# Kernel optimization log

Hardware: AMD Instinct MI355X
Metric: run time of the kernel (lower is better)

Reference implementation:

```python
import jax, jax.numpy as jnp
import numpy as np

B, E, CIN, O = 2, 50000, 8, 128


def _mesh_conv(x, gemm, w, b):
    # MeshCNN MeshConv: x (B,C,E), gemm (B,E,4) neighbor indices, w (O,C,5), b (O,)
    # gather 4 GeMM neighbors per edge, build 5 symmetric features, 1x5 conv
    neigh = jax.vmap(lambda xb, gb: xb[:, gb])(x, gemm)  # (B,C,E,4)
    f1, f2, f3, f4 = neigh[..., 0], neigh[..., 1], neigh[..., 2], neigh[..., 3]
    G = jnp.stack([x, f1 + f3, f2 + f4, jnp.abs(f1 - f3), jnp.abs(f2 - f4)], axis=-1)  # (B,C,E,5)
    return jnp.einsum('bces,ocs->boe', G, w) + b[None, :, None]


def _inorm(x, eps=1e-5):
    # InstanceNorm (no affine, biased variance) over the edge dim, per (batch, channel)
    m = jnp.mean(x, axis=-1, keepdims=True)
    v = jnp.var(x, axis=-1, keepdims=True)
    return (x - m) * jax.lax.rsqrt(v + eps)


def _conv1(x, w, b):
    # 1x1 Conv1d: x (B,C,E), w (O,C)
    return jnp.einsum('bce,oc->boe', x, w) + b[None, :, None]


def setup_inputs() -> dict:
    key = jax.random.key(0)
    ks = jax.random.split(key, 16)

    def W(k, shape, fan):
        return jax.random.normal(k, shape, jnp.float32) * np.float32(1.0 / np.sqrt(fan))

    d = {}
    d['fe'] = jax.random.normal(ks[0], (B, CIN, E), jnp.float32)
    d['gemm'] = jax.random.randint(ks[1], (B, E, 4), 0, E)
    # first-stage MeshConvs: geometry branch (5 ch) and position branch (3 ch)
    d['w_e1'] = W(ks[2], (O, 5, 5), 25);       d['b_e1'] = jnp.zeros((O,), jnp.float32)
    d['w_p1'] = W(ks[3], (O, 3, 5), 15);       d['b_p1'] = jnp.zeros((O,), jnp.float32)
    # residual-block MeshConvs (blocks=1)
    d['w_e2'] = W(ks[4], (O, O, 5), O * 5);    d['b_e2'] = jnp.zeros((O,), jnp.float32)
    d['w_p2'] = W(ks[5], (O, O, 5), O * 5);    d['b_p2'] = jnp.zeros((O,), jnp.float32)
    # Attn(in_dim=O)
    d['wa'] = W(ks[6], (O // 4, O), O);        d['ba'] = jnp.zeros((O // 4,), jnp.float32)
    d['wb'] = W(ks[7], (O // 4, O), O);        d['bb'] = jnp.zeros((O // 4,), jnp.float32)
    d['wal'] = W(ks[8], (O // 2, O // 2), O // 2);  d['bal'] = jnp.zeros((O // 2,), jnp.float32)
    d['wbl'] = W(ks[9], (O // 2, O // 2), O // 2);  d['bbl'] = jnp.zeros((O // 2,), jnp.float32)
    d['wat'] = W(ks[10], (O // 2, O // 2, 5), O // 2 * 5); d['bat'] = jnp.zeros((O // 2,), jnp.float32)
    d['wbt'] = W(ks[11], (O // 2, O // 2, 5), O // 2 * 5); d['bbt'] = jnp.zeros((O // 2,), jnp.float32)
    d['waf'] = W(ks[12], (O, O), O);           d['baf'] = jnp.zeros((O,), jnp.float32)
    d['wbf'] = W(ks[13], (O, O), O);           d['bbf'] = jnp.zeros((O,), jnp.float32)
    return d


def reference(fe, gemm, w_e1, b_e1, w_p1, b_p1, w_e2, b_e2, w_p2, b_p2,
              wa, ba, wb, bb, wal, bal, wbl, bbl, wat, bat, wbt, bbt,
              waf, baf, wbf, bbf):
    # DownConv (8-channel input path): split into edge (5) and point (3) branches
    fe_e, fe_p = fe[:, :5, :], fe[:, 5:, :]
    x1_e = jax.nn.relu(_inorm(_mesh_conv(fe_e, gemm, w_e1, b_e1)))
    x2_e = jax.nn.relu(_inorm(_mesh_conv(x1_e, gemm, w_e2, b_e2)) + x1_e)
    x1_p = jax.nn.relu(_inorm(_mesh_conv(fe_p, gemm, w_p1, b_p1)))
    x2_p = jax.nn.relu(_inorm(_mesh_conv(x1_p, gemm, w_p2, b_p2)) + x1_p)
    # Attn fusion
    x_all = jnp.concatenate([_conv1(x2_e, wa, ba), _conv1(x2_p, wb, bb)], axis=1)  # (B, O/2, E)
    x_a_two = jnp.concatenate([_conv1(x_all, wal, bal), _mesh_conv(x_all, gemm, wat, bat)], axis=1)
    x_b_two = jnp.concatenate([_conv1(x_all, wbl, bbl), _mesh_conv(x_all, gemm, wbt, bbt)], axis=1)
    wA = jax.nn.sigmoid(_inorm(_conv1(x_a_two, waf, baf)))  # (B,O,E)
    wB = jax.nn.sigmoid(_inorm(_conv1(x_b_two, wbf, bbf)))
    weights = jax.nn.softmax(jnp.stack([wA, wB], axis=1), axis=1)  # (B,2,O,E)
    agg = x2_e * weights[:, 0] + x2_p * weights[:, 1]
    # x2_ep = cat(x2_e, x2_p); also emit the attention-fused combine (before_pool)
    return jnp.concatenate([x2_e, x2_p, agg], axis=1)  # (B, 3*O, E)
```

## Files before the change

kernel.cpp:

```cpp
#include <hip/hip_runtime.h>
#include <cstdio>
#include <math.h>


#define E_TOT 50000
#define B_TOT 2
#define TILE_E 64
#define NBLK ((E_TOT + TILE_E - 1) / TILE_E)

typedef _Float16 half_t;
typedef __attribute__((ext_vector_type(4))) _Float16 h4;
typedef __attribute__((ext_vector_type(8))) _Float16 h8;
typedef __attribute__((ext_vector_type(4))) float f32x4;

__device__ __forceinline__ float sigmoidf_(float x) {
    return 1.0f / (1.0f + __expf(-x));
}
__device__ __forceinline__ h8 habs8(h8 x) {
    union { h8 h; unsigned int u[4]; } v;
    v.h = x;
#pragma unroll
    for (int i = 0; i < 4; ++i) v.u[i] &= 0x7FFF7FFFu;
    return v.h;
}

#define OFF_W1E   0
#define OFF_W1P   8192
#define OFF_WTE2  16384
#define OFF_WTP2  98304
#define OFF_WHA   180224
#define OFF_WHB   221184
#define OFF_WTA   262144
#define OFF_WTB   266240
#define OFF_WTAF  270336
#define OFF_WTBF  286720
#define WARENA_N  303104

__global__ __launch_bounds__(256)
void wprep_k(half_t* __restrict__ wa_,
             const float* __restrict__ w_e1, const float* __restrict__ w_p1,
             const float* __restrict__ w_e2, const float* __restrict__ w_p2,
             const float* __restrict__ wat,  const float* __restrict__ wbt,
             const float* __restrict__ wa,   const float* __restrict__ wb,
             const float* __restrict__ wal,  const float* __restrict__ wbl,
             const float* __restrict__ waf,  const float* __restrict__ wbf)
{
    int idx = blockIdx.x * 256 + threadIdx.x;
    switch (blockIdx.y) {
    case 0: if (idx < 8192) { int o = idx >> 6, k = idx & 63, s = k >> 3, cc = k & 7;
            float v = (s < 5 && cc < 5) ? w_e1[o * 25 + cc * 5 + s] : 0.f;
            wa_[OFF_W1E + idx] = (half_t)v; } break;
    case 1: if (idx < 8192) { int o = idx >> 6, k = idx & 63, s = k >> 3, cc = k & 7;
            float v = (s < 5 && cc >= 5) ? w_p1[o * 15 + (cc - 5) * 5 + s] : 0.f;
            wa_[OFF_W1P + idx] = (half_t)v; } break;
    case 2: if (idx < 81920) { int o = idx / 640, r = idx % 640, s = r >> 7, c = r & 127;
            wa_[OFF_WTE2 + idx] = (half_t)w_e2[(o * 128 + c) * 5 + s]; } break;
    case 3: if (idx < 81920) { int o = idx / 640, r = idx % 640, s = r >> 7, c = r & 127;
            wa_[OFF_WTP2 + idx] = (half_t)w_p2[(o * 128 + c) * 5 + s]; } break;
    case 4: if (idx < 40960) { int o = idx / 320, r = idx % 320, s = r >> 6, c = r & 63;
            float v = (o < 64) ? (s == 0 ? wal[o * 64 + c] : 0.f)
                               : wat[((o - 64) * 64 + c) * 5 + s];
            wa_[OFF_WHA + idx] = (half_t)v; } break;
    case 5: if (idx < 40960) { int o = idx / 320, r = idx % 320, s = r >> 6, c = r & 63;
            float v = (o < 64) ? (s == 0 ? wbl[o * 64 + c] : 0.f)
                               : wbt[((o - 64) * 64 + c) * 5 + s];
            wa_[OFF_WHB + idx] = (half_t)v; } break;
    case 6: if (idx < 4096)  wa_[OFF_WTA  + idx] = (half_t)wa[idx];  break;
    case 7: if (idx < 4096)  wa_[OFF_WTB  + idx] = (half_t)wb[idx];  break;
    case 8: if (idx < 16384) wa_[OFF_WTAF + idx] = (half_t)waf[idx]; break;
    case 9: if (idx < 16384) wa_[OFF_WTBF + idx] = (half_t)wbf[idx]; break;
    }
}

__global__ __launch_bounds__(256)
void transpose_in_k(const float* __restrict__ fe, float* __restrict__ fet)
{
    int b = blockIdx.z;
    int e = blockIdx.x * 256 + threadIdx.x;
    if (e >= E_TOT) return;
    float v[8];
#pragma unroll
    for (int c = 0; c < 8; ++c)
        v[c] = fe[((long)b * 8 + c) * E_TOT + e];
    float4* dst = (float4*)&fet[((long)b * E_TOT + e) * 8];
    dst[0] = make_float4(v[0], v[1], v[2], v[3]);
    dst[1] = make_float4(v[4], v[5], v[6], v[7]);
}

__global__ __launch_bounds__(512)
void mesh1_both_k(const float* __restrict__ fet, const int* __restrict__ gemm,
                  const half_t* __restrict__ war,
                  const float* __restrict__ be1, const float* __restrict__ bp1,
                  half_t* __restrict__ tmpe, half_t* __restrict__ tmpp,
                  float* __restrict__ parte, float* __restrict__ partp)
{
    __shared__ h8 Gl[64 * 8];
    __shared__ int nidx[64][4];

    const int tid  = threadIdx.x;
    const int b    = blockIdx.y;
    const int e0   = blockIdx.x * TILE_E;
    const int lane = tid & 63;
    const int wv   = tid >> 6;
    const int l15  = lane & 15;
    const int kg   = lane >> 4;
    const int br   = wv >> 2;
    const int o0   = (wv & 3) * 32;

    const float* xb = fet + (long)b * E_TOT * 8;

    if (tid < 256) {
        int e = tid >> 2, s = tid & 3;
        int eg = e0 + e;
        nidx[e][s] = (eg < E_TOT) ? gemm[((long)b * E_TOT + eg) * 4 + s] : 0;
    }
    __syncthreads();

    {
        int e = tid >> 3, g = tid & 7;
        int eg = e0 + e;
        int se = (eg < E_TOT) ? eg : 0;
        h8 r;
        if (g == 0) {
            const float* p = xb + (long)se * 8;
            float4 v0 = *(const float4*)p, v1 = *(const float4*)(p + 4);
            r[0] = (half_t)v0.x; r[1] = (half_t)v0.y; r[2] = (half_t)v0.z; r[3] = (half_t)v0.w;
            r[4] = (half_t)v1.x; r[5] = (half_t)v1.y; r[6] = (half_t)v1.z; r[7] = (half_t)v1.w;
        } else if (g <= 4) {
            int ia = (g == 1 || g == 3) ? 0 : 1;
            const float* pa = xb + (long)nidx[e][ia] * 8;
            const float* pb = xb + (long)nidx[e][ia + 2] * 8;
            float4 a0 = *(const float4*)pa, a1 = *(const float4*)(pa + 4);
            float4 b0 = *(const float4*)pb, b1 = *(const float4*)(pb + 4);
            float aa[8] = {a0.x, a0.y, a0.z, a0.w, a1.x, a1.y, a1.z, a1.w};
            float bb[8] = {b0.x, b0.y, b0.z, b0.w, b1.x, b1.y, b1.z, b1.w};
            if (g <= 2) {
#pragma unroll
                for (int j = 0; j < 8; ++j) r[j] = (half_t)(aa[j] + bb[j]);
            } else {
#pragma unroll
                for (int j = 0; j < 8; ++j) r[j] = (half_t)fabsf(aa[j] - bb[j]);
            }
        } else {
#pragma unroll
            for (int j = 0; j < 8; ++j) r[j] = (half_t)0.f;
        }
        Gl[(e * 8 + g) ^ (e & 7)] = r;
    }
    __syncthreads();

    f32x4 acc[4][2];
#pragma unroll
    for (int mt = 0; mt < 4; ++mt)
#pragma unroll
        for (int nt = 0; nt < 2; ++nt)
#pragma unroll
            for (int j = 0; j < 4; ++j) acc[mt][nt][j] = 0.f;

    const half_t* wt = war + (br ? OFF_W1P : OFF_W1E);
#pragma unroll
    for (int ks = 0; ks < 2; ++ks) {
        h8 bw[2];
#pragma unroll
        for (int nt = 0; nt < 2; ++nt)
            bw[nt] = *(const h8*)(wt + (long)(o0 + nt * 16 + l15) * 64 + ks * 32 + kg * 8);
#pragma unroll
        for (int mt = 0; mt < 4; ++mt) {
            int row = mt * 16 + l15;
            h8 a = Gl[row * 8 + ((ks * 4 + kg) ^ (row & 7))];
#pragma unroll
            for (int nt = 0; nt < 2; ++nt)
                acc[mt][nt] = __builtin_amdgcn_mfma_f32_16x16x32_f16(a, bw[nt], acc[mt][nt], 0, 0, 0);
        }
    }

    const float* bias = br ? bp1 : be1;
    half_t* yb = (br ? tmpp : tmpe) + (long)b * E_TOT * 128;
    float* part = br ? partp : parte;
    float bv[2], s1[2], s2[2];
#pragma unroll
    for (int nt = 0; nt < 2; ++nt) {
        bv[nt] = bias[o0 + nt * 16 + l15];
        s1[nt] = 0.f; s2[nt] = 0.f;
    }
#pragma unroll
    for (int mt = 0; mt < 4; ++mt) {
        int ebase = e0 + mt * 16 + (kg << 2);
#pragma unroll
        for (int j = 0; j < 4; ++j) {
            if (ebase + j < E_TOT) {
#pragma unroll
                for (int nt = 0; nt < 2; ++nt) {
                    float v = acc[mt][nt][j] + bv[nt];
                    yb[(long)(ebase + j) * 128 + o0 + nt * 16 + l15] = (half_t)v;
                    s1[nt] += v; s2[nt] += v * v;
                }
            }
        }
    }
#pragma unroll
    for (int nt = 0; nt < 2; ++nt) {
        s1[nt] += __shfl_xor(s1[nt], 16); s1[nt] += __shfl_xor(s1[nt], 32);
        s2[nt] += __shfl_xor(s2[nt], 16); s2[nt] += __shfl_xor(s2[nt], 32);
    }
    if (lane < 16) {
        long pb = ((long)b * NBLK + blockIdx.x) * 128;
#pragma unroll
        for (int nt = 0; nt < 2; ++nt) {
            part[(pb + o0 + nt * 16 + lane) * 2 + 0] = s1[nt];
            part[(pb + o0 + nt * 16 + lane) * 2 + 1] = s2[nt];
        }
    }
}

__global__ __launch_bounds__(512)
void mesh2_k(const half_t* __restrict__ x1e, const half_t* __restrict__ x1p,
             const int* __restrict__ gemm, const half_t* __restrict__ war,
             const float* __restrict__ be, const float* __restrict__ bp,
             half_t* __restrict__ tmpe, half_t* __restrict__ tmpp,
             float* __restrict__ parte, float* __restrict__ partp)
{
    __shared__ h8 GlA[64 * 16];
    __shared__ h8 GlB[64 * 16];
    __shared__ int nidx[64][4];

    const int tid  = threadIdx.x;
    const int br   = blockIdx.y;
    const int b    = blockIdx.z;
    const int e0   = blockIdx.x * TILE_E;
    const int lane = tid & 63;
    const int wv   = tid >> 6;
    const int l15  = lane & 15;
    const int kg   = lane >> 4;
    const int o0   = wv * 16;

    const half_t* xb = (br ? x1p : x1e) + (long)b * E_TOT * 128;
    const half_t* wt = war + (br ? OFF_WTP2 : OFF_WTE2);

    if (tid < 256) {
        int e = tid >> 2, s = tid & 3;
        int eg = e0 + e;
        nidx[e][s] = (eg < E_TOT) ? gemm[((long)b * E_TOT + eg) * 4 + s] : 0;
    }

    auto stage_self = [&](h8* dst) {
#pragma unroll
        for (int t = 0; t < 2; ++t) {
            int q = t * 512 + tid;
            int e = q >> 4, c8 = q & 15;
            int eg = e0 + e;
            int se = (eg < E_TOT) ? eg : 0;
            dst[(e * 16 + c8) ^ (e & 7)] = *(const h8*)(xb + (long)se * 128 + c8 * 8);
        }
    };
    auto stage_pair = [&](h8* dstS, h8* dstD, int ia, int ib) {
#pragma unroll
        for (int t = 0; t < 2; ++t) {
            int q = t * 512 + tid;
            int e = q >> 4, c8 = q & 15;
            int na = nidx[e][ia], nb = nidx[e][ib];
            h8 a  = *(const h8*)(xb + (long)na * 128 + c8 * 8);
            h8 bq = *(const h8*)(xb + (long)nb * 128 + c8 * 8);
            int slot = (e * 16 + c8) ^ (e & 7);
            dstS[slot] = a + bq;
            dstD[slot] = habs8(a - bq);
        }
    };

    f32x4 acc[4];
#pragma unroll
    for (int mt = 0; mt < 4; ++mt)
#pragma unroll
        for (int j = 0; j < 4; ++j) acc[mt][j] = 0.f;

    auto compute_chunk = [&](const h8* buf, int s) {
#pragma unroll
        for (int ks = 0; ks < 4; ++ks) {
            h8 bw = *(const h8*)(wt + ((long)(o0 + l15) * 5 + s) * 128 + ks * 32 + kg * 8);
#pragma unroll
            for (int mt = 0; mt < 4; ++mt) {
                int row = mt * 16 + l15;
                h8 a = buf[row * 16 + ((ks * 4 + kg) ^ (row & 7))];
                acc[mt] = __builtin_amdgcn_mfma_f32_16x16x32_f16(a, bw, acc[mt], 0, 0, 0);
            }
        }
    };

    stage_self(GlA);
    __syncthreads();
    compute_chunk(GlA, 0);
    __syncthreads();
    stage_pair(GlA, GlB, 0, 2);
    __syncthreads();
    compute_chunk(GlA, 1);
    compute_chunk(GlB, 3);
    __syncthreads();
    stage_pair(GlA, GlB, 1, 3);
    __syncthreads();
    compute_chunk(GlA, 2);
    compute_chunk(GlB, 4);

    const float* bias = br ? bp : be;
    half_t* yb = (br ? tmpp : tmpe) + (long)b * E_TOT * 128;
    float* part = br ? partp : parte;
    float bv = bias[o0 + l15];
    float s1 = 0.f, s2 = 0.f;
#pragma unroll
    for (int mt = 0; mt < 4; ++mt) {
        int ebase = e0 + mt * 16 + (kg << 2);
#pragma unroll
        for (int j = 0; j < 4; ++j) {
            if (ebase + j < E_TOT) {
                float v = acc[mt][j] + bv;
                yb[(long)(ebase + j) * 128 + o0 + l15] = (half_t)v;
                s1 += v; s2 += v * v;
            }
        }
    }
    s1 += __shfl_xor(s1, 16); s1 += __shfl_xor(s1, 32);
    s2 += __shfl_xor(s2, 16); s2 += __shfl_xor(s2, 32);
    if (lane < 16) {
        long pb = ((long)b * NBLK + blockIdx.x) * 128;
        part[(pb + o0 + lane) * 2 + 0] = s1;
        part[(pb + o0 + lane) * 2 + 1] = s2;
    }
}

__global__ __launch_bounds__(512)
void heads_gates_k(const half_t* __restrict__ xall, const int* __restrict__ gemm,
                   const half_t* __restrict__ war,
                   const float* __restrict__ bal, const float* __restrict__ bbl,
                   const float* __restrict__ bat, const float* __restrict__ bbt,
                   const float* __restrict__ baf, const float* __restrict__ bbf,
                   half_t* __restrict__ tmpe, half_t* __restrict__ tmpp,
                   float* __restrict__ parte, float* __restrict__ partp)
{
    __shared__ h8 arena[2048];
    __shared__ int nidx[64][4];

    const int tid  = threadIdx.x;
    const int b    = blockIdx.y;
    const int e0   = blockIdx.x * TILE_E;
    const int lane = tid & 63;
    const int wv   = tid >> 6;
    const int hd   = wv >> 2;
    const int o0   = (wv & 3) * 32;
    const int l15  = lane & 15;
    const int kg   = lane >> 4;

    h8* C0 = arena;
    h8* C1 = arena + 512;
    h8* C2 = arena + 1024;

    const half_t* xb = xall + (long)b * E_TOT * 64;

    if (tid < 256) {
        int e = tid >> 2, s = tid & 3;
        int eg = e0 + e;
        nidx[e][s] = (eg < E_TOT) ? gemm[((long)b * E_TOT + eg) * 4 + s] : 0;
    }
    __syncthreads();

    const int te = tid >> 3, tc = tid & 7;
    const int tslot = (te * 8 + tc) ^ (te & 7);

    {
        int eg = e0 + te;
        int se = (eg < E_TOT) ? eg : 0;
        C0[tslot] = *(const h8*)(xb + (long)se * 64 + tc * 8);
    }
    h8 rA, rB;
    {
        rA = *(const h8*)(xb + (long)nidx[te][0] * 64 + tc * 8);
        rB = *(const h8*)(xb + (long)nidx[te][2] * 64 + tc * 8);
    }
    __syncthreads();

    f32x4 acc[4][2];
#pragma unroll
    for (int mt = 0; mt < 4; ++mt)
#pragma unroll
        for (int nt = 0; nt < 2; ++nt)
#pragma unroll
            for (int j = 0; j < 4; ++j) acc[mt][nt][j] = 0.f;

    const half_t* wt = war + (hd ? OFF_WHB : OFF_WHA);
    auto chunk = [&](const h8* buf, int s) {
#pragma unroll
        for (int ks = 0; ks < 2; ++ks) {
            h8 bw0 = *(const h8*)(wt + ((long)(o0 + l15) * 5 + s) * 64 + ks * 32 + kg * 8);
            h8 bw1 = *(const h8*)(wt + ((long)(o0 + 16 + l15) * 5 + s) * 64 + ks * 32 + kg * 8);
#pragma unroll
            for (int mt = 0; mt < 4; ++mt) {
                int row = mt * 16 + l15;
                h8 a = buf[row * 8 + ((ks * 4 + kg) ^ (row & 7))];
                acc[mt][0] = __builtin_amdgcn_mfma_f32_16x16x32_f16(a, bw0, acc[mt][0], 0, 0, 0);
                acc[mt][1] = __builtin_amdgcn_mfma_f32_16x16x32_f16(a, bw1, acc[mt][1], 0, 0, 0);
            }
        }
    };

    chunk(C0, 0);
    __syncthreads();
    {
        C1[tslot] = rA + rB;
        C2[tslot] = habs8(rA - rB);
        rA = *(const h8*)(xb + (long)nidx[te][1] * 64 + tc * 8);
        rB = *(const h8*)(xb + (long)nidx[te][3] * 64 + tc * 8);
    }
    __syncthreads();
    chunk(C1, 1);
    chunk(C2, 3);
    __syncthreads();
    {
        C1[tslot] = rA + rB;
        C2[tslot] = habs8(rA - rB);
    }
    __syncthreads();
    chunk(C1, 2);
    chunk(C2, 4);
    __syncthreads();

    {
        half_t* X = (half_t*)(arena + hd * 1024);
        float bv[2];
#pragma unroll
        for (int nt = 0; nt < 2; ++nt) {
            int o = o0 + nt * 16 + l15;
            bv[nt] = (o < 64) ? (hd ? bbl[o] : bal[o]) : (hd ? bbt[o - 64] : bat[o - 64]);
        }
#pragma unroll
        for (int mt = 0; mt < 4; ++mt) {
#pragma unroll
            for (int j = 0; j < 4; ++j) {
                int e = mt * 16 + (kg << 2) + j;
#pragma unroll
                for (int nt = 0; nt < 2; ++nt) {
                    int c = o0 + nt * 16 + l15;
                    int slot = (e * 16 + (c >> 3)) ^ (e & 7);
                    X[slot * 8 + (c & 7)] = (half_t)(acc[mt][nt][j] + bv[nt]);
                }
            }
        }
    }
    __syncthreads();

    f32x4 g[4][2];
#pragma unroll
    for (int mt = 0; mt < 4; ++mt)
#pragma unroll
        for (int nt = 0; nt < 2; ++nt)
#pragma unroll
            for (int j = 0; j < 4; ++j) g[mt][nt][j] = 0.f;

    const half_t* wtg = war + (hd ? OFF_WTBF : OFF_WTAF);
    const h8* X = arena + hd * 1024;
#pragma unroll
    for (int ks = 0; ks < 4; ++ks) {
        h8 bw0 = *(const h8*)(wtg + (long)(o0 + l15) * 128 + ks * 32 + kg * 8);
        h8 bw1 = *(const h8*)(wtg + (long)(o0 + 16 + l15) * 128 + ks * 32 + kg * 8);
#pragma unroll
        for (int mt = 0; mt < 4; ++mt) {
            int row = mt * 16 + l15;
            h8 a = X[row * 16 + ((ks * 4 + kg) ^ (row & 7))];
            g[mt][0] = __builtin_amdgcn_mfma_f32_16x16x32_f16(a, bw0, g[mt][0], 0, 0, 0);
            g[mt][1] = __builtin_amdgcn_mfma_f32_16x16x32_f16(a, bw1, g[mt][1], 0, 0, 0);
        }
    }

    const float* biasg = hd ? bbf : baf;
    half_t* yb = (hd ? tmpp : tmpe) + (long)b * E_TOT * 128;
    float* part = hd ? partp : parte;
    float bg[2] = {biasg[o0 + l15], biasg[o0 + 16 + l15]};
    float s1[2] = {0.f, 0.f}, s2[2] = {0.f, 0.f};
#pragma unroll
    for (int mt = 0; mt < 4; ++mt) {
        int ebase = e0 + mt * 16 + (kg << 2);
#pragma unroll
        for (int j = 0; j < 4; ++j) {
            if (ebase + j < E_TOT) {
#pragma unroll
                for (int nt = 0; nt < 2; ++nt) {
                    float v = g[mt][nt][j] + bg[nt];
                    yb[(long)(ebase + j) * 128 + o0 + nt * 16 + l15] = (half_t)v;
                    s1[nt] += v; s2[nt] += v * v;
                }
            }
        }
    }
#pragma unroll
    for (int nt = 0; nt < 2; ++nt) {
        s1[nt] += __shfl_xor(s1[nt], 16); s1[nt] += __shfl_xor(s1[nt], 32);
        s2[nt] += __shfl_xor(s2[nt], 16); s2[nt] += __shfl_xor(s2[nt], 32);
    }
    if (lane < 16) {
        long pb = ((long)b * NBLK + blockIdx.x) * 128;
#pragma unroll
        for (int nt = 0; nt < 2; ++nt) {
            part[(pb + o0 + nt * 16 + lane) * 2 + 0] = s1[nt];
            part[(pb + o0 + nt * 16 + lane) * 2 + 1] = s2[nt];
        }
    }
}

__global__ __launch_bounds__(256)
void xall_k(const half_t* __restrict__ x2e, const half_t* __restrict__ x2p,
            const half_t* __restrict__ war,
            const float* __restrict__ ba, const float* __restrict__ bb,
            half_t* __restrict__ xall)
{
    __shared__ h8 Gl[64 * 16];

    const int tid  = threadIdx.x;
    const int br   = blockIdx.y;
    const int b    = blockIdx.z;
    const int e0   = blockIdx.x * TILE_E;
    const int lane = tid & 63;
    const int wv   = tid >> 6;
    const int l15  = lane & 15;
    const int kg   = lane >> 4;
    const int eoff = wv * 16;

    const half_t* xb = (br ? x2p : x2e) + (long)b * E_TOT * 128;
    const half_t* wt = war + (br ? OFF_WTB : OFF_WTA);

#pragma unroll
    for (int t = 0; t < 4; ++t) {
        int q = t * 256 + tid;
        int e = q >> 4, c8 = q & 15;
        int eg = e0 + e;
        int se = (eg < E_TOT) ? eg : 0;
        Gl[(e * 16 + c8) ^ (e & 7)] = *(const h8*)(xb + (long)se * 128 + c8 * 8);
    }
    __syncthreads();

    f32x4 acc[2];
#pragma unroll
    for (int nt = 0; nt < 2; ++nt)
#pragma unroll
        for (int j = 0; j < 4; ++j) acc[nt][j] = 0.f;

#pragma unroll
    for (int ks = 0; ks < 4; ++ks) {
        h8 bw[2];
#pragma unroll
        for (int nt = 0; nt < 2; ++nt)
            bw[nt] = *(const h8*)(wt + (long)(nt * 16 + l15) * 128 + ks * 32 + kg * 8);
        int row = eoff + l15;
        h8 a = Gl[row * 16 + ((ks * 4 + kg) ^ (row & 7))];
#pragma unroll
        for (int nt = 0; nt < 2; ++nt)
            acc[nt] = __builtin_amdgcn_mfma_f32_16x16x32_f16(a, bw[nt], acc[nt], 0, 0, 0);
    }

    const float* bias = br ? bb : ba;
    half_t* yb = xall + (long)b * E_TOT * 64;
    int oOff = br * 32;
#pragma unroll
    for (int nt = 0; nt < 2; ++nt) {
        float bv = bias[nt * 16 + l15];
        int ebase = e0 + eoff + (kg << 2);
#pragma unroll
        for (int j = 0; j < 4; ++j) {
            if (ebase + j < E_TOT)
                yb[(long)(ebase + j) * 64 + oOff + nt * 16 + l15] = (half_t)(acc[nt][j] + bv);
        }
    }
}

__global__ __launch_bounds__(256)
void stats2_k(const float* __restrict__ parte, const float* __restrict__ partp,
              float* __restrict__ statse, float* __restrict__ statsp)
{
    int g = blockIdx.x;
    int br = g >> 8, rem = g & 255, b = rem >> 7, o = rem & 127;
    const float* part = br ? partp : parte;
    float* stats = br ? statsp : statse;
    int tid = threadIdx.x;
    float s1 = 0.f, s2 = 0.f;
    for (int k = tid; k < NBLK; k += 256) {
        long base = (((long)b * NBLK + k) * 128 + o) * 2;
        s1 += part[base];
        s2 += part[base + 1];
    }
#pragma unroll
    for (int d = 1; d < 64; d <<= 1) {
        s1 += __shfl_xor(s1, d);
        s2 += __shfl_xor(s2, d);
    }
    __shared__ float r1[4], r2[4];
    int wv = tid >> 6;
    if ((tid & 63) == 0) { r1[wv] = s1; r2[wv] = s2; }
    __syncthreads();
    if (tid == 0) {
        s1 = r1[0] + r1[1] + r1[2] + r1[3];
        s2 = r2[0] + r2[1] + r2[2] + r2[3];
        float mean = s1 / (float)E_TOT;
        float var  = s2 / (float)E_TOT - mean * mean;
        var = fmaxf(var, 0.f);
        stats[(b * 128 + o) * 2 + 0] = mean;
        stats[(b * 128 + o) * 2 + 1] = rsqrtf(var + 1e-5f);
    }
}

__global__ __launch_bounds__(256)
void norm_act2_k(const half_t* __restrict__ tmpe, const half_t* __restrict__ tmpp,
                 const float* __restrict__ statse, const float* __restrict__ statsp,
                 half_t* __restrict__ x1e, half_t* __restrict__ x1p)
{
    const long PER = (long)B_TOT * E_TOT * 16;
    long q = (long)blockIdx.x * 256 + threadIdx.x;
    if (q >= 2 * PER) return;
    int br = (q >= PER);
    q -= (long)br * PER;
    const half_t* src = br ? tmpp : tmpe;
    const float* stats = br ? statsp : statse;
    half_t* dst = br ? x1p : x1e;
    long idx = q * 8;
    int c = (int)(idx & 127);
    int b = (int)((idx >> 7) / E_TOT);
    h8 v = *(const h8*)&src[idx];
    h8 r;
#pragma unroll
    for (int j = 0; j < 8; ++j) {
        float2 st = *(const float2*)&stats[(b * 128 + c + j) * 2];
        float t = ((float)v[j] - st.x) * st.y;
        r[j] = (half_t)fmaxf(t, 0.f);
    }
    *(h8*)&dst[idx] = r;
}

__global__ __launch_bounds__(256)
void normres2_k(const half_t* __restrict__ tmpe, const half_t* __restrict__ tmpp,
                const half_t* __restrict__ x1e, const half_t* __restrict__ x1p,
                const float* __restrict__ statse, const float* __restrict__ statsp,
                float* __restrict__ outb,
                half_t* __restrict__ x2e, half_t* __restrict__ x2p)
{
    __shared__ float T[32 * 68];
    int br = blockIdx.y >> 2, cg = blockIdx.y & 3;
    int b = blockIdx.z;
    int e0 = blockIdx.x * 64;
    int tid = threadIdx.x;
    const half_t* xin = br ? tmpp : tmpe;
    const half_t* res = br ? x1p : x1e;
    const float* stats = br ? statsp : statse;
    half_t* x2b = br ? x2p : x2e;
    int sect = br * 128;
#pragma unroll
    for (int i = 0; i < 2; ++i) {
        int q = tid + i * 256;
        int e = q >> 3, cq = q & 7;
        int eg = e0 + e;
        int se = (eg < E_TOT) ? eg : (E_TOT - 1);
        int c = cg * 32 + cq * 4;
        long base = ((long)b * E_TOT + se) * 128 + c;
        h4 v4 = *(const h4*)&xin[base];
        h4 r4 = *(const h4*)&res[base];
        h4 o4;
#pragma unroll
        for (int j = 0; j < 4; ++j) {
            float2 st = *(const float2*)&stats[(b * 128 + c + j) * 2];
            float t = ((float)v4[j] - st.x) * st.y + (float)r4[j];
            t = fmaxf(t, 0.f);
            T[(cq * 4 + j) * 68 + e] = t;
            o4[j] = (half_t)t;
        }
        if (eg < E_TOT) *(h4*)&x2b[base] = o4;
    }
    __syncthreads();
#pragma unroll
    for (int i = 0; i < 2; ++i) {
        int q = tid + i * 256;
        int cl = q >> 4, eq = q & 15;
        int e4 = e0 + eq * 4;
        int cglob = sect + cg * 32 + cl;
        float4 v = *(const float4*)&T[cl * 68 + eq * 4];
        long obase = ((long)b * 384 + cglob) * E_TOT + e4;
        if (e4 + 3 < E_TOT) {
            *(float4*)&outb[obase] = v;
        } else {
            const float* vp = &v.x;
            for (int j = 0; j < 4; ++j)
                if (e4 + j < E_TOT) outb[obase + j] = vp[j];
        }
    }
}

__global__ __launch_bounds__(256)
void gate_agg2_k(const half_t* __restrict__ tA, const half_t* __restrict__ tB,
                 const float* __restrict__ statsA, const float* __restrict__ statsB,
                 const half_t* __restrict__ x2e, const half_t* __restrict__ x2p,
                 float* __restrict__ outb)
{
    __shared__ float T[32 * 68];
    int b = blockIdx.z, cg = blockIdx.y;
    int e0 = blockIdx.x * 64;
    int tid = threadIdx.x;
#pragma unroll
    for (int i = 0; i < 2; ++i) {
        int q = tid + i * 256;
        int e = q >> 3, cq = q & 7;
        int eg = e0 + e;
        int se = (eg < E_TOT) ? eg : (E_TOT - 1);
        int c = cg * 32 + cq * 4;
        long base = ((long)b * E_TOT + se) * 128 + c;
        h4 a4 = *(const h4*)&tA[base];
        h4 b4 = *(const h4*)&tB[base];
        h4 xe4 = *(const h4*)&x2e[base];
        h4 xp4 = *(const h4*)&x2p[base];
#pragma unroll
        for (int j = 0; j < 4; ++j) {
            float2 sa = *(const float2*)&statsA[(b * 128 + c + j) * 2];
            float2 sb = *(const float2*)&statsB[(b * 128 + c + j) * 2];
            float na = sigmoidf_(((float)a4[j] - sa.x) * sa.y);
            float nb = sigmoidf_(((float)b4[j] - sb.x) * sb.y);
            float s = sigmoidf_(na - nb);
            T[(cq * 4 + j) * 68 + e] = (float)xe4[j] * s + (float)xp4[j] * (1.f - s);
        }
    }
    __syncthreads();
#pragma unroll
    for (int i = 0; i < 2; ++i) {
        int q = tid + i * 256;
        int cl = q >> 4, eq = q & 15;
        int e4 = e0 + eq * 4;
        int cglob = cg * 32 + cl;
        float4 v = *(const float4*)&T[cl * 68 + eq * 4];
        long ab = ((long)b * 384 + 256 + cglob) * E_TOT + e4;
        if (e4 + 3 < E_TOT) {
            *(float4*)&outb[ab] = v;
        } else {
            const float* vp = &v.x;
            for (int j = 0; j < 4; ++j)
                if (e4 + j < E_TOT) outb[ab + j] = vp[j];
        }
    }
}

extern "C" void kernel_launch(void* const* d_in, const int* in_sizes, int n_in,
                              void* d_out, int out_size, void* d_ws, size_t ws_size,
                              hipStream_t stream)
{
    const float* fe   = (const float*)d_in[0];
    const int*   gemm = (const int*)  d_in[1];
    const float* w_e1 = (const float*)d_in[2];  const float* b_e1 = (const float*)d_in[3];
    const float* w_p1 = (const float*)d_in[4];  const float* b_p1 = (const float*)d_in[5];
    const float* w_e2 = (const float*)d_in[6];  const float* b_e2 = (const float*)d_in[7];
    const float* w_p2 = (const float*)d_in[8];  const float* b_p2 = (const float*)d_in[9];
    const float* wa   = (const float*)d_in[10]; const float* ba   = (const float*)d_in[11];
    const float* wb   = (const float*)d_in[12]; const float* bb   = (const float*)d_in[13];
    const float* wal  = (const float*)d_in[14]; const float* bal  = (const float*)d_in[15];
    const float* wbl  = (const float*)d_in[16]; const float* bbl  = (const float*)d_in[17];
    const float* wat  = (const float*)d_in[18]; const float* bat  = (const float*)d_in[19];
    const float* wbt  = (const float*)d_in[20]; const float* bbt  = (const float*)d_in[21];
    const float* waf  = (const float*)d_in[22]; const float* baf  = (const float*)d_in[23];
    const float* wbf  = (const float*)d_in[24]; const float* bbf  = (const float*)d_in[25];
    float* out = (float*)d_out;

    const long EB = (long)E_TOT;

    char* wp = (char*)d_ws;
    auto alloc = [&](size_t bytes) -> void* {
        void* r = (void*)wp;
        wp += (bytes + 255) & ~(size_t)255;
        return r;
    };
    float*  FET    = (float*)alloc((size_t)B_TOT * EB * 8 * 4);
    half_t* TMP_E  = (half_t*)alloc((size_t)B_TOT * EB * 128 * 2);
    half_t* TMP_P  = (half_t*)alloc((size_t)B_TOT * EB * 128 * 2);
    half_t* X1E    = (half_t*)alloc((size_t)B_TOT * EB * 128 * 2);
    half_t* X1P    = (half_t*)alloc((size_t)B_TOT * EB * 128 * 2);
    half_t* X2E    = (half_t*)alloc((size_t)B_TOT * EB * 128 * 2);
    half_t* X2P    = (half_t*)alloc((size_t)B_TOT * EB * 128 * 2);
    half_t* XALL   = (half_t*)alloc((size_t)B_TOT * EB * 64 * 2);
    float*  PART_E = (float*)alloc((size_t)B_TOT * NBLK * 128 * 2 * 4);
    float*  PART_P = (float*)alloc((size_t)B_TOT * NBLK * 128 * 2 * 4);
    float*  STATSE = (float*)alloc((size_t)B_TOT * 128 * 2 * 4);
    float*  STATSP = (float*)alloc((size_t)B_TOT * 128 * 2 * 4);
    half_t* WAR    = (half_t*)alloc((size_t)WARENA_N * 2);

    if ((size_t)(wp - (char*)d_ws) > ws_size) {
        fprintf(stderr, "kernel_launch: ws too small (%zu < %zu)\n",
                ws_size, (size_t)(wp - (char*)d_ws));
        return;
    }

    dim3 blk256(256), blk512(512);
    dim3 gI(NBLK, B_TOT);
    dim3 gE2(NBLK, 2, B_TOT);
    dim3 gT((E_TOT + 255) / 256, 1, B_TOT);
    dim3 gN8(NBLK, 8, B_TOT);
    dim3 gN4(NBLK, 4, B_TOT);
    int gA2 = (int)((2 * (long)B_TOT * EB * 16 + 255) / 256);

    wprep_k<<<dim3(320, 10, 1), blk256, 0, stream>>>(WAR,
        w_e1, w_p1, w_e2, w_p2, wat, wbt, wa, wb, wal, wbl, waf, wbf);
    transpose_in_k<<<gT, blk256, 0, stream>>>(fe, FET);

    mesh1_both_k<<<gI, blk512, 0, stream>>>(FET, gemm, WAR, b_e1, b_p1,
        TMP_E, TMP_P, PART_E, PART_P);
    stats2_k<<<512, blk256, 0, stream>>>(PART_E, PART_P, STATSE, STATSP);
    norm_act2_k<<<gA2, blk256, 0, stream>>>(TMP_E, TMP_P, STATSE, STATSP, X1E, X1P);

    mesh2_k<<<gE2, blk512, 0, stream>>>(X1E, X1P, gemm, WAR, b_e2, b_p2,
        TMP_E, TMP_P, PART_E, PART_P);
    stats2_k<<<512, blk256, 0, stream>>>(PART_E, PART_P, STATSE, STATSP);
    normres2_k<<<gN8, blk256, 0, stream>>>(TMP_E, TMP_P, X1E, X1P, STATSE, STATSP,
        out, X2E, X2P);

    xall_k<<<gE2, blk256, 0, stream>>>(X2E, X2P, WAR, ba, bb, XALL);

    heads_gates_k<<<gI, blk512, 0, stream>>>(XALL, gemm, WAR,
        bal, bbl, bat, bbt, baf, bbf, TMP_E, TMP_P, PART_E, PART_P);

    stats2_k<<<512, blk256, 0, stream>>>(PART_E, PART_P, STATSE, STATSP);
    gate_agg2_k<<<gN4, blk256, 0, stream>>>(TMP_E, TMP_P, STATSE, STATSP,
        X2E, X2P, out);
}
```

Measured before the change: 345.9 us.

## Fuse instance-norm application into mesh2 gather and normres with xall conv

```diff
diff --git a/kernel.cpp b/kernel.cpp
--- a/kernel.cpp
+++ b/kernel.cpp
@@ -7,6 +7,7 @@
 #define B_TOT 2
 #define TILE_E 64
 #define NBLK ((E_TOT + TILE_E - 1) / TILE_E)
+#define TPAD 67
 
 typedef _Float16 half_t;
 typedef __attribute__((ext_vector_type(4))) _Float16 h4;
@@ -22,6 +23,17 @@
 #pragma unroll
     for (int i = 0; i < 4; ++i) v.u[i] &= 0x7FFF7FFFu;
     return v.h;
+}
+__device__ __forceinline__ h8 hmax0(h8 x) {
+#if defined(__has_builtin) && __has_builtin(__builtin_elementwise_max)
+    h8 z = {};
+    return __builtin_elementwise_max(x, z);
+#else
+    h8 r;
+#pragma unroll
+    for (int j = 0; j < 8; ++j) r[j] = (x[j] > (half_t)0) ? x[j] : (half_t)0;
+    return r;
+#endif
 }
 
 #define OFF_W1E   0
@@ -214,10 +226,11 @@
 }
 
 __global__ __launch_bounds__(512)
-void mesh2_k(const half_t* __restrict__ x1e, const half_t* __restrict__ x1p,
+void mesh2_k(const half_t* __restrict__ tmp1e, const half_t* __restrict__ tmp1p,
+             const half_t* __restrict__ statshe, const half_t* __restrict__ statshp,
              const int* __restrict__ gemm, const half_t* __restrict__ war,
              const float* __restrict__ be, const float* __restrict__ bp,
-             half_t* __restrict__ tmpe, half_t* __restrict__ tmpp,
+             half_t* __restrict__ tmp2e, half_t* __restrict__ tmp2p,
              float* __restrict__ parte, float* __restrict__ partp)
 {
     __shared__ h8 GlA[64 * 16];
@@ -234,14 +247,21 @@
     const int kg   = lane >> 4;
     const int o0   = wv * 16;
 
-    const half_t* xb = (br ? x1p : x1e) + (long)b * E_TOT * 128;
+    const half_t* xb = (br ? tmp1p : tmp1e) + (long)b * E_TOT * 128;
+    const half_t* sh = (br ? statshp : statshe) + (long)b * 256;
     const half_t* wt = war + (br ? OFF_WTP2 : OFF_WTE2);
+
+    const int tc0 = tid & 15;
+    const h8 sc8 = *(const h8*)(sh + tc0 * 8);
+    const h8 sf8 = *(const h8*)(sh + 128 + tc0 * 8);
 
     if (tid < 256) {
         int e = tid >> 2, s = tid & 3;
         int eg = e0 + e;
         nidx[e][s] = (eg < E_TOT) ? gemm[((long)b * E_TOT + eg) * 4 + s] : 0;
     }
+
+    auto nrm = [&](h8 v) -> h8 { return hmax0(v * sc8 + sf8); };
 
     auto stage_self = [&](h8* dst) {
 #pragma unroll
@@ -250,7 +270,7 @@
             int e = q >> 4, c8 = q & 15;
             int eg = e0 + e;
             int se = (eg < E_TOT) ? eg : 0;
-            dst[(e * 16 + c8) ^ (e & 7)] = *(const h8*)(xb + (long)se * 128 + c8 * 8);
+            dst[(e * 16 + c8) ^ (e & 7)] = nrm(*(const h8*)(xb + (long)se * 128 + c8 * 8));
         }
     };
     auto stage_pair = [&](h8* dstS, h8* dstD, int ia, int ib) {
@@ -259,8 +279,8 @@
             int q = t * 512 + tid;
             int e = q >> 4, c8 = q & 15;
             int na = nidx[e][ia], nb = nidx[e][ib];
-            h8 a  = *(const h8*)(xb + (long)na * 128 + c8 * 8);
-            h8 bq = *(const h8*)(xb + (long)nb * 128 + c8 * 8);
+            h8 a  = nrm(*(const h8*)(xb + (long)na * 128 + c8 * 8));
+            h8 bq = nrm(*(const h8*)(xb + (long)nb * 128 + c8 * 8));
             int slot = (e * 16 + c8) ^ (e & 7);
             dstS[slot] = a + bq;
             dstD[slot] = habs8(a - bq);
@@ -301,7 +321,7 @@
     compute_chunk(GlB, 4);
 
     const float* bias = br ? bp : be;
-    half_t* yb = (br ? tmpp : tmpe) + (long)b * E_TOT * 128;
+    half_t* yb = (br ? tmp2p : tmp2e) + (long)b * E_TOT * 128;
     float* part = br ? partp : parte;
     float bv = bias[o0 + l15];
     float s1 = 0.f, s2 = 0.f;
@@ -327,12 +347,105 @@
 }
 
 __global__ __launch_bounds__(512)
+void normres_xall_k(const half_t* __restrict__ tmp2e, const half_t* __restrict__ tmp2p,
+                    const half_t* __restrict__ tmp1e, const half_t* __restrict__ tmp1p,
+                    const half_t* __restrict__ sh1e, const half_t* __restrict__ sh1p,
+                    const half_t* __restrict__ sh2e, const half_t* __restrict__ sh2p,
+                    const half_t* __restrict__ war,
+                    const float* __restrict__ ba, const float* __restrict__ bb,
+                    float* __restrict__ outb,
+                    half_t* __restrict__ x2e, half_t* __restrict__ x2p,
+                    half_t* __restrict__ xall)
+{
+    __shared__ float Tf[128 * TPAD];
+    __shared__ h8 X2t[1024];
+
+    const int tid  = threadIdx.x;
+    const int br   = blockIdx.y;
+    const int b    = blockIdx.z;
+    const int e0   = blockIdx.x * TILE_E;
+    const int lane = tid & 63;
+    const int wv   = tid >> 6;
+    const int l15  = lane & 15;
+    const int kg   = lane >> 4;
+
+    const half_t* t2 = (br ? tmp2p : tmp2e) + (long)b * E_TOT * 128;
+    const half_t* t1 = (br ? tmp1p : tmp1e) + (long)b * E_TOT * 128;
+    const half_t* s1p = (br ? sh1p : sh1e) + (long)b * 256;
+    const half_t* s2p = (br ? sh2p : sh2e) + (long)b * 256;
+    half_t* x2g = (br ? x2p : x2e) + (long)b * E_TOT * 128;
+
+    const int tc0 = tid & 15;
+    const h8 sc1 = *(const h8*)(s1p + tc0 * 8);
+    const h8 sf1 = *(const h8*)(s1p + 128 + tc0 * 8);
+    const h8 sc2 = *(const h8*)(s2p + tc0 * 8);
+    const h8 sf2 = *(const h8*)(s2p + 128 + tc0 * 8);
+
+#pragma unroll
+    for (int t = 0; t < 2; ++t) {
+        int q = t * 512 + tid;
+        int e = q >> 4;
+        int eg = e0 + e;
+        int se = (eg < E_TOT) ? eg : (E_TOT - 1);
+        h8 v2 = *(const h8*)(t2 + (long)se * 128 + tc0 * 8);
+        h8 v1 = *(const h8*)(t1 + (long)se * 128 + tc0 * 8);
+        h8 x1 = hmax0(v1 * sc1 + sf1);
+        h8 x2 = hmax0(v2 * sc2 + sf2 + x1);
+        X2t[(e * 16 + tc0) ^ (e & 7)] = x2;
+        if (eg < E_TOT) *(h8*)(x2g + (long)eg * 128 + tc0 * 8) = x2;
+#pragma unroll
+        for (int j = 0; j < 8; ++j)
+            Tf[(tc0 * 8 + j) * TPAD + e] = (float)x2[j];
+    }
+    __syncthreads();
+
+#pragma unroll
+    for (int i = 0; i < 4; ++i) {
+        int task = i * 512 + tid;
+        int cl = task >> 4, eq = task & 15;
+        int e4 = e0 + eq * 4;
+        float4 v = *(const float4*)&Tf[cl * TPAD + eq * 4];
+        int cglob = br * 128 + cl;
+        long obase = ((long)b * 384 + cglob) * E_TOT + e4;
+        if (e4 + 3 < E_TOT) {
+            *(float4*)&outb[obase] = v;
+        } else {
+            const float* vp = &v.x;
+            for (int j = 0; j < 4; ++j)
+                if (e4 + j < E_TOT) outb[obase + j] = vp[j];
+        }
+    }
+
+    const int eoff = (wv & 3) * 16;
+    const int og   = wv >> 2;
+    const half_t* wt = war + (br ? OFF_WTB : OFF_WTA);
+    f32x4 acc;
+#pragma unroll
+    for (int j = 0; j < 4; ++j) acc[j] = 0.f;
+#pragma unroll
+    for (int ks = 0; ks < 4; ++ks) {
+        h8 bw = *(const h8*)(wt + (long)(og * 16 + l15) * 128 + ks * 32 + kg * 8);
+        int row = eoff + l15;
+        h8 a = X2t[row * 16 + ((ks * 4 + kg) ^ (row & 7))];
+        acc = __builtin_amdgcn_mfma_f32_16x16x32_f16(a, bw, acc, 0, 0, 0);
+    }
+    float bv = (br ? bb : ba)[og * 16 + l15];
+    half_t* yall = xall + (long)b * E_TOT * 64;
+#pragma unroll
+    for (int j = 0; j < 4; ++j) {
+        int e = e0 + eoff + (kg << 2) + j;
+        if (e < E_TOT)
+            yall[(long)e * 64 + br * 32 + og * 16 + l15] = (half_t)(acc[j] + bv);
+    }
+}
+
+__global__ __launch_bounds__(512)
 void heads_gates_k(const half_t* __restrict__ xall, const int* __restrict__ gemm,
                    const half_t* __restrict__ war,
                    const float* __restrict__ bal, const float* __restrict__ bbl,
                    const float* __restrict__ bat, const float* __restrict__ bbt,
                    const float* __restrict__ baf, const float* __restrict__ bbf,
-                   half_t* __restrict__ tmpe, half_t* __restrict__ tmpp,
+                   half_t* __restrict__ gA, half_t* __restrict__ gB,
                    float* __restrict__ parte, float* __restrict__ partp)
 {
     __shared__ h8 arena[2048];
@@ -469,7 +582,7 @@
     }
 
     const float* biasg = hd ? bbf : baf;
-    half_t* yb = (hd ? tmpp : tmpe) + (long)b * E_TOT * 128;
+    half_t* yb = (hd ? gB : gA) + (long)b * E_TOT * 128;
     float* part = hd ? partp : parte;
     float bg[2] = {biasg[o0 + l15], biasg[o0 + 16 + l15]};
     float s1[2] = {0.f, 0.f}, s2[2] = {0.f, 0.f};
@@ -504,78 +617,15 @@
 }
 
 __global__ __launch_bounds__(256)
-void xall_k(const half_t* __restrict__ x2e, const half_t* __restrict__ x2p,
-            const half_t* __restrict__ war,
-            const float* __restrict__ ba, const float* __restrict__ bb,
-            half_t* __restrict__ xall)
-{
-    __shared__ h8 Gl[64 * 16];
-
-    const int tid  = threadIdx.x;
-    const int br   = blockIdx.y;
-    const int b    = blockIdx.z;
-    const int e0   = blockIdx.x * TILE_E;
-    const int lane = tid & 63;
-    const int wv   = tid >> 6;
-    const int l15  = lane & 15;
-    const int kg   = lane >> 4;
-    const int eoff = wv * 16;
-
-    const half_t* xb = (br ? x2p : x2e) + (long)b * E_TOT * 128;
-    const half_t* wt = war + (br ? OFF_WTB : OFF_WTA);
-
-#pragma unroll
-    for (int t = 0; t < 4; ++t) {
-        int q = t * 256 + tid;
-        int e = q >> 4, c8 = q & 15;
-        int eg = e0 + e;
-        int se = (eg < E_TOT) ? eg : 0;
-        Gl[(e * 16 + c8) ^ (e & 7)] = *(const h8*)(xb + (long)se * 128 + c8 * 8);
-    }
-    __syncthreads();
-
-    f32x4 acc[2];
-#pragma unroll
-    for (int nt = 0; nt < 2; ++nt)
-#pragma unroll
-        for (int j = 0; j < 4; ++j) acc[nt][j] = 0.f;
-
-#pragma unroll
-    for (int ks = 0; ks < 4; ++ks) {
-        h8 bw[2];
-#pragma unroll
-        for (int nt = 0; nt < 2; ++nt)
-            bw[nt] = *(const h8*)(wt + (long)(nt * 16 + l15) * 128 + ks * 32 + kg * 8);
-        int row = eoff + l15;
-        h8 a = Gl[row * 16 + ((ks * 4 + kg) ^ (row & 7))];
-#pragma unroll
-        for (int nt = 0; nt < 2; ++nt)
-            acc[nt] = __builtin_amdgcn_mfma_f32_16x16x32_f16(a, bw[nt], acc[nt], 0, 0, 0);
-    }
-
-    const float* bias = br ? bb : ba;
-    half_t* yb = xall + (long)b * E_TOT * 64;
-    int oOff = br * 32;
-#pragma unroll
-    for (int nt = 0; nt < 2; ++nt) {
-        float bv = bias[nt * 16 + l15];
-        int ebase = e0 + eoff + (kg << 2);
-#pragma unroll
-        for (int j = 0; j < 4; ++j) {
-            if (ebase + j < E_TOT)
-                yb[(long)(ebase + j) * 64 + oOff + nt * 16 + l15] = (half_t)(acc[nt][j] + bv);
-        }
-    }
-}
-
-__global__ __launch_bounds__(256)
 void stats2_k(const float* __restrict__ parte, const float* __restrict__ partp,
-              float* __restrict__ statse, float* __restrict__ statsp)
+              float* __restrict__ statse, float* __restrict__ statsp,
+              half_t* __restrict__ statshe, half_t* __restrict__ statshp)
 {
     int g = blockIdx.x;
     int br = g >> 8, rem = g & 255, b = rem >> 7, o = rem & 127;
     const float* part = br ? partp : parte;
     float* stats = br ? statsp : statse;
+    half_t* statsh = br ? statshp : statshe;
     int tid = threadIdx.x;
     float s1 = 0.f, s2 = 0.f;
     for (int k = tid; k < NBLK; k += 256) {
@@ -598,92 +648,11 @@
         float mean = s1 / (float)E_TOT;
         float var  = s2 / (float)E_TOT - mean * mean;
         var = fmaxf(var, 0.f);
+        float rstd = rsqrtf(var + 1e-5f);
         stats[(b * 128 + o) * 2 + 0] = mean;
-        stats[(b * 128 + o) * 2 + 1] = rsqrtf(var + 1e-5f);
-    }
-}
-
-__global__ __launch_bounds__(256)
-void norm_act2_k(const half_t* __restrict__ tmpe, const half_t* __restrict__ tmpp,
-                 const float* __restrict__ statse, const float* __restrict__ statsp,
-                 half_t* __restrict__ x1e, half_t* __restrict__ x1p)
-{
-    const long PER = (long)B_TOT * E_TOT * 16;
-    long q = (long)blockIdx.x * 256 + threadIdx.x;
-    if (q >= 2 * PER) return;
-    int br = (q >= PER);
-    q -= (long)br * PER;
-    const half_t* src = br ? tmpp : tmpe;
-    const float* stats = br ? statsp : statse;
-    half_t* dst = br ? x1p : x1e;
-    long idx = q * 8;
-    int c = (int)(idx & 127);
-    int b = (int)((idx >> 7) / E_TOT);
-    h8 v = *(const h8*)&src[idx];
-    h8 r;
-#pragma unroll
-    for (int j = 0; j < 8; ++j) {
-        float2 st = *(const float2*)&stats[(b * 128 + c + j) * 2];
-        float t = ((float)v[j] - st.x) * st.y;
-        r[j] = (half_t)fmaxf(t, 0.f);
-    }
-    *(h8*)&dst[idx] = r;
-}
-
-__global__ __launch_bounds__(256)
-void normres2_k(const half_t* __restrict__ tmpe, const half_t* __restrict__ tmpp,
-                const half_t* __restrict__ x1e, const half_t* __restrict__ x1p,
-                const float* __restrict__ statse, const float* __restrict__ statsp,
-                float* __restrict__ outb,
-                half_t* __restrict__ x2e, half_t* __restrict__ x2p)
-{
-    __shared__ float T[32 * 68];
-    int br = blockIdx.y >> 2, cg = blockIdx.y & 3;
-    int b = blockIdx.z;
-    int e0 = blockIdx.x * 64;
-    int tid = threadIdx.x;
-    const half_t* xin = br ? tmpp : tmpe;
-    const half_t* res = br ? x1p : x1e;
-    const float* stats = br ? statsp : statse;
-    half_t* x2b = br ? x2p : x2e;
-    int sect = br * 128;
-#pragma unroll
-    for (int i = 0; i < 2; ++i) {
-        int q = tid + i * 256;
-        int e = q >> 3, cq = q & 7;
-        int eg = e0 + e;
-        int se = (eg < E_TOT) ? eg : (E_TOT - 1);
-        int c = cg * 32 + cq * 4;
-        long base = ((long)b * E_TOT + se) * 128 + c;
-        h4 v4 = *(const h4*)&xin[base];
-        h4 r4 = *(const h4*)&res[base];
-        h4 o4;
-#pragma unroll
-        for (int j = 0; j < 4; ++j) {
-            float2 st = *(const float2*)&stats[(b * 128 + c + j) * 2];
-            float t = ((float)v4[j] - st.x) * st.y + (float)r4[j];
-            t = fmaxf(t, 0.f);
-            T[(cq * 4 + j) * 68 + e] = t;
-            o4[j] = (half_t)t;
-        }
-        if (eg < E_TOT) *(h4*)&x2b[base] = o4;
-    }
-    __syncthreads();
-#pragma unroll
-    for (int i = 0; i < 2; ++i) {
-        int q = tid + i * 256;
-        int cl = q >> 4, eq = q & 15;
-        int e4 = e0 + eq * 4;
-        int cglob = sect + cg * 32 + cl;
-        float4 v = *(const float4*)&T[cl * 68 + eq * 4];
-        long obase = ((long)b * 384 + cglob) * E_TOT + e4;
-        if (e4 + 3 < E_TOT) {
-            *(float4*)&outb[obase] = v;
-        } else {
-            const float* vp = &v.x;
-            for (int j = 0; j < 4; ++j)
-                if (e4 + j < E_TOT) outb[obase + j] = vp[j];
-        }
+        stats[(b * 128 + o) * 2 + 1] = rstd;
+        statsh[b * 256 + o]       = (half_t)rstd;
+        statsh[b * 256 + 128 + o] = (half_t)(-mean * rstd);
     }
 }
 
@@ -767,10 +736,10 @@
         return r;
     };
     float*  FET    = (float*)alloc((size_t)B_TOT * EB * 8 * 4);
-    half_t* TMP_E  = (half_t*)alloc((size_t)B_TOT * EB * 128 * 2);
-    half_t* TMP_P  = (half_t*)alloc((size_t)B_TOT * EB * 128 * 2);
-    half_t* X1E    = (half_t*)alloc((size_t)B_TOT * EB * 128 * 2);
-    half_t* X1P    = (half_t*)alloc((size_t)B_TOT * EB * 128 * 2);
+    half_t* TMP1_E = (half_t*)alloc((size_t)B_TOT * EB * 128 * 2);
+    half_t* TMP1_P = (half_t*)alloc((size_t)B_TOT * EB * 128 * 2);
+    half_t* TMP2_E = (half_t*)alloc((size_t)B_TOT * EB * 128 * 2);
+    half_t* TMP2_P = (half_t*)alloc((size_t)B_TOT * EB * 128 * 2);
     half_t* X2E    = (half_t*)alloc((size_t)B_TOT * EB * 128 * 2);
     half_t* X2P    = (half_t*)alloc((size_t)B_TOT * EB * 128 * 2);
     half_t* XALL   = (half_t*)alloc((size_t)B_TOT * EB * 64 * 2);
@@ -778,6 +747,10 @@
     float*  PART_P = (float*)alloc((size_t)B_TOT * NBLK * 128 * 2 * 4);
     float*  STATSE = (float*)alloc((size_t)B_TOT * 128 * 2 * 4);
     float*  STATSP = (float*)alloc((size_t)B_TOT * 128 * 2 * 4);
+    half_t* SH1E   = (half_t*)alloc((size_t)B_TOT * 256 * 2);
+    half_t* SH1P   = (half_t*)alloc((size_t)B_TOT * 256 * 2);
+    half_t* SH2E   = (half_t*)alloc((size_t)B_TOT * 256 * 2);
+    half_t* SH2P   = (half_t*)alloc((size_t)B_TOT * 256 * 2);
     half_t* WAR    = (half_t*)alloc((size_t)WARENA_N * 2);
 
     if ((size_t)(wp - (char*)d_ws) > ws_size) {
@@ -790,31 +763,27 @@
     dim3 gI(NBLK, B_TOT);
     dim3 gE2(NBLK, 2, B_TOT);
     dim3 gT((E_TOT + 255) / 256, 1, B_TOT);
-    dim3 gN8(NBLK, 8, B_TOT);
     dim3 gN4(NBLK, 4, B_TOT);
-    int gA2 = (int)((2 * (long)B_TOT * EB * 16 + 255) / 256);
 
     wprep_k<<<dim3(320, 10, 1), blk256, 0, stream>>>(WAR,
         w_e1, w_p1, w_e2, w_p2, wat, wbt, wa, wb, wal, wbl, waf, wbf);
     transpose_in_k<<<gT, blk256, 0, stream>>>(fe, FET);
 
     mesh1_both_k<<<gI, blk512, 0, stream>>>(FET, gemm, WAR, b_e1, b_p1,
-        TMP_E, TMP_P, PART_E, PART_P);
-    stats2_k<<<512, blk256, 0, stream>>>(PART_E, PART_P, STATSE, STATSP);
-    norm_act2_k<<<gA2, blk256, 0, stream>>>(TMP_E, TMP_P, STATSE, STATSP, X1E, X1P);
-
-    mesh2_k<<<gE2, blk512, 0, stream>>>(X1E, X1P, gemm, WAR, b_e2, b_p2,
-        TMP_E, TMP_P, PART_E, PART_P);
-    stats2_k<<<512, blk256, 0, stream>>>(PART_E, PART_P, STATSE, STATSP);
-    normres2_k<<<gN8, blk256, 0, stream>>>(TMP_E, TMP_P, X1E, X1P, STATSE, STATSP,
-        out, X2E, X2P);
-
-    xall_k<<<gE2, blk256, 0, stream>>>(X2E, X2P, WAR, ba, bb, XALL);
+        TMP1_E, TMP1_P, PART_E, PART_P);
+    stats2_k<<<512, blk256, 0, stream>>>(PART_E, PART_P, STATSE, STATSP, SH1E, SH1P);
+
+    mesh2_k<<<gE2, blk512, 0, stream>>>(TMP1_E, TMP1_P, SH1E, SH1P, gemm, WAR,
+        b_e2, b_p2, TMP2_E, TMP2_P, PART_E, PART_P);
+    stats2_k<<<512, blk256, 0, stream>>>(PART_E, PART_P, STATSE, STATSP, SH2E, SH2P);
+
+    normres_xall_k<<<gE2, blk512, 0, stream>>>(TMP2_E, TMP2_P, TMP1_E, TMP1_P,
+        SH1E, SH1P, SH2E, SH2P, WAR, ba, bb, out, X2E, X2P, XALL);
 
     heads_gates_k<<<gI, blk512, 0, stream>>>(XALL, gemm, WAR,
-        bal, bbl, bat, bbt, baf, bbf, TMP_E, TMP_P, PART_E, PART_P);
-
-    stats2_k<<<512, blk256, 0, stream>>>(PART_E, PART_P, STATSE, STATSP);
-    gate_agg2_k<<<gN4, blk256, 0, stream>>>(TMP_E, TMP_P, STATSE, STATSP,
+        bal, bbl, bat, bbt, baf, bbf, TMP1_E, TMP1_P, PART_E, PART_P);
+    stats2_k<<<512, blk256, 0, stream>>>(PART_E, PART_P, STATSE, STATSP, SH1E, SH1P);
+
+    gate_agg2_k<<<gN4, blk256, 0, stream>>>(TMP1_E, TMP1_P, STATSE, STATSP,
         X2E, X2P, out);
 }
```

After: 309.3 us. -10.6%, faster.
